# Kernel tuning notes

Measured on AMD Instinct MI355X. Metric: run time of the kernel, lower is better.

## Reference

```python
import jax, jax.numpy as jnp
import numpy as np

K_TOP = 64  # top-k selection size (init kwarg k)


def setup_inputs() -> dict:
    key = jax.random.key(0)
    k1, k2, k3, k4 = jax.random.split(key, 4)
    N, M, D = 512, 100000, 1024
    queries = jax.random.normal(k1, (N, D), dtype=jnp.float32)
    keys = jax.random.normal(k2, (M, D), dtype=jnp.float32)
    values = jax.random.normal(k3, (M, D), dtype=jnp.float32)
    affine = jax.random.normal(k4, (D,), dtype=jnp.float32)  # diag affine param (low_parameter=True)
    return {"queries": queries, "keys": keys, "values": values, "affine": affine}


def reference(queries, keys, values, affine):
    # low_parameter=True -> weight matrix is diag(affine): (queries @ diag(a)) == queries * a
    # scores[n, m] = (queries * affine) @ keys.T ; reduce max over queries dim (dim=0)
    scores = jnp.max(jnp.einsum('nd,md->nm', queries * affine, keys), axis=0)  # [M]
    weights, indices = jax.lax.top_k(scores, K_TOP)            # [k], [k]
    w = jax.nn.softmax(weights)                                # softmax over the k selected scores
    encoding = jnp.sum(w[:, None] * values[indices], axis=0)   # [V]
    return encoding, indices
```

## Files before the change

kernel.cpp:

```cpp
#include <hip/hip_runtime.h>
#include <cstdint>
#include <cstddef>


typedef __attribute__((ext_vector_type(8))) short bf16x8;
typedef __attribute__((ext_vector_type(4))) float f32x4;

static constexpr int NQ = 512;
static constexpr int DD = 1024;
static constexpr int MK = 100000;
static constexpr int BM = 64;
static constexpr int BK = 64;
static constexpr int NKS = DD / BK;
static constexpr int MBLOCKS = (MK + BM - 1) / BM;
static constexpr int CAP = 1024;

static constexpr size_t KSTAGE_OFF   = 0;
static constexpr size_t KSTAGE_BYTES = (size_t)MBLOCKS * NKS * BM * 128;
static constexpr size_t QSTAGE_OFF   = KSTAGE_OFF + KSTAGE_BYTES;
static constexpr size_t QSTAGE_BYTES = (size_t)NKS * NQ * 128;
static constexpr size_t SCORES_OFF   = QSTAGE_OFF + QSTAGE_BYTES;
static constexpr size_t SCORES_BYTES = (size_t)MBLOCKS * BM * sizeof(float);
static constexpr size_t CIDX_OFF     = SCORES_OFF + SCORES_BYTES;
static constexpr size_t RESC_OFF     = CIDX_OFF + (size_t)CAP * 4;
static constexpr size_t CNT_OFF      = RESC_OFF + (size_t)CAP * 4;
static constexpr size_t HIST_OFF     = CNT_OFF + 64;
static constexpr size_t VLO_OFF      = HIST_OFF + 8192 * 4;

static constexpr int AOFF = 0;
static constexpr int BOFF = 8192;
static constexpr int GEMM_LDS = 8192 + 65536;

static __device__ __forceinline__ unsigned short f32_to_bf16_rne(float f) {
    unsigned int u = __float_as_uint(f);
    unsigned int r = (u + 0x7FFFu + ((u >> 16) & 1u)) >> 16;
    return (unsigned short)r;
}
static __device__ __forceinline__ unsigned int xform(float f) {
    unsigned int u = __float_as_uint(f);
    return u ^ ((unsigned int)((int)u >> 31) | 0x80000000u);
}
static __device__ __forceinline__ float unxform(unsigned int u) {
    unsigned int b = (u & 0x80000000u) ? (u ^ 0x80000000u) : ~u;
    return __uint_as_float(b);
}

typedef __attribute__((address_space(1))) const unsigned int g1u32;
typedef __attribute__((address_space(3))) unsigned int l3u32;
static __device__ __forceinline__ void async16(const void* g, void* l) {
    __builtin_amdgcn_global_load_lds((g1u32*)g, (l3u32*)(uintptr_t)l, 16, 0, 0);
}

__global__ void prep_q(const float* __restrict__ q, const float* __restrict__ a,
                       unsigned short* __restrict__ qs) {
    int id  = blockIdx.x * 256 + threadIdx.x;
    int p   = id & 7;
    int row = (id >> 3) & (NQ - 1);
    int ks  = id >> 12;
    int c   = p ^ (row & 7);
    int kb  = ks * BK + c * 8;

    const float* qrow = q + (size_t)row * DD + kb;
    float4 v0 = *(const float4*)(qrow);
    float4 v1 = *(const float4*)(qrow + 4);
    float4 a0 = *(const float4*)(a + kb);
    float4 a1 = *(const float4*)(a + kb + 4);
    float f[8] = {v0.x * a0.x, v0.y * a0.y, v0.z * a0.z, v0.w * a0.w,
                  v1.x * a1.x, v1.y * a1.y, v1.z * a1.z, v1.w * a1.w};
    bf16x8 o;
#pragma unroll
    for (int j = 0; j < 8; ++j) o[j] = (short)f32_to_bf16_rne(f[j]);
    *(bf16x8*)(qs + (size_t)id * 8) = o;
}

__global__ void prep_keys(const float* __restrict__ keys,
                          unsigned short* __restrict__ kst) {
    size_t id = (size_t)blockIdx.x * 256 + threadIdx.x;
    int p   = (int)(id & 7);
    int row = (int)((id >> 3) & 63);
    int ks  = (int)((id >> 9) & 15);
    int mb  = (int)(id >> 13);
    int gm  = mb * 64 + row;
    bf16x8 o;
    if (gm < MK) {
        int col = ks * BK + (p ^ (row & 7)) * 8;
        const float* src = keys + (size_t)gm * DD + col;
        float4 v0 = *(const float4*)(src);
        float4 v1 = *(const float4*)(src + 4);
        float f[8] = {v0.x, v0.y, v0.z, v0.w, v1.x, v1.y, v1.z, v1.w};
#pragma unroll
        for (int j = 0; j < 8; ++j) o[j] = (short)f32_to_bf16_rne(f[j]);
    } else {
#pragma unroll
        for (int j = 0; j < 8; ++j) o[j] = 0;
    }
    *(bf16x8*)(kst + id * 8) = o;
}

__launch_bounds__(512, 4)
__global__ void scores_gemm(const unsigned short* __restrict__ kstage,
                            const unsigned short* __restrict__ qs,
                            float* __restrict__ scores) {
    extern __shared__ char smem[];
    const int tid  = threadIdx.x;
    const int wid  = tid >> 6;
    const int lane = tid & 63;
    const int g    = lane >> 4;
    const int r16  = lane & 15;

    const int nwg = gridDim.x;
    const int qq  = nwg >> 3, rr = nwg & 7;
    const int xcd = blockIdx.x & 7, loc = blockIdx.x >> 3;
    const int mb  = (xcd < rr ? xcd * (qq + 1) : rr * (qq + 1) + (xcd - rr) * qq) + loc;
    const int m0  = mb * BM;

    const char* asrc = (const char*)kstage + ((size_t)mb * NKS) * 8192
                     + wid * 1024 + lane * 16;
    const char* bsrc = (const char*)qs + (size_t)(wid * 64) * 128 + (size_t)lane * 16;

    int aoff[2][4], boff[2][4];
#pragma unroll
    for (int s = 0; s < 2; ++s) {
#pragma unroll
        for (int rt = 0; rt < 4; ++rt) {
            int row = rt * 16 + r16;
            aoff[s][rt] = AOFF + row * 128 + (((s * 4 + g) ^ (row & 7)) << 4);
        }
#pragma unroll
        for (int ct = 0; ct < 4; ++ct) {
            int row = wid * 64 + ct * 16 + r16;
            boff[s][ct] = BOFF + row * 128 + (((s * 4 + g) ^ (row & 7)) << 4);
        }
    }

    f32x4 acc[4][4] = {};

    for (int ks = 0; ks < NKS; ++ks) {
        async16(asrc + (size_t)ks * 8192, smem + AOFF + wid * 1024);
#pragma unroll
        for (int i = 0; i < 8; ++i)
            async16(bsrc + (size_t)ks * 65536 + i * 1024,
                    smem + BOFF + wid * 8192 + i * 1024);
        __syncthreads();

#pragma unroll
        for (int s = 0; s < 2; ++s) {
            bf16x8 ah[4], bh[4];
#pragma unroll
            for (int rt = 0; rt < 4; ++rt) ah[rt] = *(const bf16x8*)(smem + aoff[s][rt]);
#pragma unroll
            for (int ct = 0; ct < 4; ++ct) bh[ct] = *(const bf16x8*)(smem + boff[s][ct]);
#pragma unroll
            for (int rt = 0; rt < 4; ++rt)
#pragma unroll
                for (int ct = 0; ct < 4; ++ct)
                    acc[rt][ct] = __builtin_amdgcn_mfma_f32_16x16x32_bf16(ah[rt], bh[ct], acc[rt][ct], 0, 0, 0);
        }
        __syncthreads();
    }

    float* wmax = (float*)smem;
#pragma unroll
    for (int rt = 0; rt < 4; ++rt) {
#pragma unroll
        for (int r = 0; r < 4; ++r) {
            float mx = acc[rt][0][r];
            mx = fmaxf(mx, acc[rt][1][r]);
            mx = fmaxf(mx, acc[rt][2][r]);
            mx = fmaxf(mx, acc[rt][3][r]);
#pragma unroll
            for (int off = 1; off < 16; off <<= 1)
                mx = fmaxf(mx, __shfl_xor(mx, off));
            if (r16 == 0) wmax[wid * 64 + rt * 16 + g * 4 + r] = mx;
        }
    }
    __syncthreads();
    if (tid < BM) {
        float mx = wmax[tid];
#pragma unroll
        for (int w = 1; w < 8; ++w) mx = fmaxf(mx, wmax[w * 64 + tid]);
        int gm = m0 + tid;
        if (gm < MK) scores[gm] = mx;
    }
}

__global__ void zero_hist(unsigned int* __restrict__ hist, int* __restrict__ cnt) {
    int i = blockIdx.x * 1024 + threadIdx.x;
    if (i < 8192) hist[i] = 0;
    if (i == 0) cnt[0] = 0;
}

__global__ void hist_build(const float* __restrict__ scores, unsigned int* __restrict__ hist) {
    __shared__ unsigned int lh[8192];
    for (int i = threadIdx.x; i < 8192; i += 256) lh[i] = 0;
    __syncthreads();
    for (int i = blockIdx.x * 256 + threadIdx.x; i < MK; i += gridDim.x * 256)
        atomicAdd(&lh[xform(scores[i]) >> 19], 1u);
    __syncthreads();
    for (int i = threadIdx.x; i < 8192; i += 256) {
        unsigned int c = lh[i];
        if (c) atomicAdd(&hist[i], c);
    }
}

__launch_bounds__(1024)
__global__ void find_thresh(const unsigned int* __restrict__ hist, float* __restrict__ vlo) {
    __shared__ unsigned int s0[1024], s1[1024];
    const int tid = threadIdx.x;
    unsigned int s = 0;
#pragma unroll
    for (int j = 0; j < 8; ++j) s += hist[tid * 8 + j];
    s0[tid] = s;
    __syncthreads();
    unsigned int* src = s0;
    unsigned int* dst = s1;
    for (int off = 1; off < 1024; off <<= 1) {
        unsigned int v = src[tid] + ((tid + off < 1024) ? src[tid + off] : 0u);
        __syncthreads();
        dst[tid] = v;
        __syncthreads();
        unsigned int* t = src; src = dst; dst = t;
    }
    unsigned int suf  = src[tid];
    unsigned int sufn = (tid < 1023) ? src[tid + 1] : 0u;
    if (suf >= 64u && sufn < 64u) {
        unsigned int acc = sufn;
        int b = tid * 8 + 7;
        for (;; --b) { acc += hist[b]; if (acc >= 64u) break; }
        vlo[0] = unxform(((unsigned int)b) << 19) - 1.0f;
    }
}

__global__ void collect(const float* __restrict__ scores, const float* __restrict__ vlo,
                        int* __restrict__ cidx, int* __restrict__ cnt) {
    const float t = vlo[0];
    for (int i = blockIdx.x * 256 + threadIdx.x; i < MK; i += gridDim.x * 256) {
        if (scores[i] >= t) {
            int p = atomicAdd(cnt, 1);
            if (p < CAP) cidx[p] = i;
        }
    }
}

__launch_bounds__(256)
__global__ void rescore(const float* __restrict__ q, const float* __restrict__ a,
                        const float* __restrict__ keys,
                        const int* __restrict__ cidx, const int* __restrict__ cnt,
                        float* __restrict__ resc) {
    __shared__ float w[1024];
    __shared__ float smax[4];
    const int b = blockIdx.x;
    if (b >= cnt[0]) return;
    const int m   = cidx[b];
    const int tid = threadIdx.x;

    for (int d = tid; d < 1024; d += 256) w[d] = a[d] * keys[(size_t)m * DD + d];
    __syncthreads();

    const int wid = tid >> 6, lane = tid & 63;
    float best = -__builtin_inff();
    for (int n = wid; n < NQ; n += 4) {
        const float* qr = q + (size_t)n * DD;
        float p = 0.f;
#pragma unroll
        for (int j = 0; j < 4; ++j) {
            float4 v  = *(const float4*)(qr + lane * 4 + 256 * j);
            float4 ww = *(const float4*)(&w[lane * 4 + 256 * j]);
            p += v.x * ww.x + v.y * ww.y + v.z * ww.z + v.w * ww.w;
        }
#pragma unroll
        for (int off = 1; off < 64; off <<= 1) p += __shfl_xor(p, off);
        best = fmaxf(best, p);
    }
    if (lane == 0) smax[wid] = best;
    __syncthreads();
    if (tid == 0)
        resc[b] = fmaxf(fmaxf(smax[0], smax[1]), fmaxf(smax[2], smax[3]));
}

__launch_bounds__(256)
__global__ void final_select(const int* __restrict__ cidx, const float* __restrict__ resc,
                             const int* __restrict__ cnt, const float* __restrict__ values,
                             float* __restrict__ out) {
    __shared__ float selw[64];
    __shared__ int   seli[64];
    const int tid = threadIdx.x;
    int nc = cnt[0];
    if (nc > CAP) nc = CAP;

    if (tid < 64) {
        const int lane = tid;
        float lv[16]; int li[16];
#pragma unroll
        for (int j = 0; j < 16; ++j) {
            int slot = lane + 64 * j;
            bool ok = slot < nc;
            lv[j] = ok ? resc[slot] : -__builtin_inff();
            li[j] = ok ? cidx[slot] : 0x7fffffff;
        }
        for (int it = 0; it < 64; ++it) {
            float bv = -__builtin_inff();
            int bg = 0x7fffffff, bj = 0;
#pragma unroll
            for (int j = 0; j < 16; ++j)
                if (lv[j] > bv || (lv[j] == bv && li[j] < bg)) { bv = lv[j]; bg = li[j]; bj = j; }
            int bcode = (lane << 4) | bj;
#pragma unroll
            for (int off = 1; off < 64; off <<= 1) {
                float ov = __shfl_xor(bv, off);
                int   og = __shfl_xor(bg, off);
                int   oc = __shfl_xor(bcode, off);
                if (ov > bv || (ov == bv && og < bg)) { bv = ov; bg = og; bcode = oc; }
            }
            if ((bcode >> 4) == lane) {
                int wj = bcode & 15;
#pragma unroll
                for (int j = 0; j < 16; ++j) if (j == wj) lv[j] = -__builtin_inff();
            }
            if (lane == 0) { selw[it] = bv; seli[it] = bg; }
        }
    }
    __syncthreads();

    if (tid < 64) {
        float x = selw[tid];
        float mx = x;
#pragma unroll
        for (int off = 1; off < 64; off <<= 1) mx = fmaxf(mx, __shfl_xor(mx, off));
        float e = expf(x - mx);
        float s = e;
#pragma unroll
        for (int off = 1; off < 64; off <<= 1) s += __shfl_xor(s, off);
        selw[tid] = e / s;
        out[DD + tid] = (float)seli[tid];
    }
    __syncthreads();

    for (int d = tid; d < DD; d += 256) {
        float accv = 0.f;
        for (int i = 0; i < 64; ++i)
            accv += selw[i] * values[(size_t)seli[i] * DD + d];
        out[d] = accv;
    }
}

extern "C" void kernel_launch(void* const* d_in, const int* in_sizes, int n_in,
                              void* d_out, int out_size, void* d_ws, size_t ws_size,
                              hipStream_t stream) {
    (void)in_sizes; (void)n_in; (void)out_size; (void)ws_size;
    const float* queries = (const float*)d_in[0];
    const float* keys    = (const float*)d_in[1];
    const float* values  = (const float*)d_in[2];
    const float* affine  = (const float*)d_in[3];
    float* out = (float*)d_out;
    char*  ws  = (char*)d_ws;

    unsigned short* kstage = (unsigned short*)(ws + KSTAGE_OFF);
    unsigned short* qstage = (unsigned short*)(ws + QSTAGE_OFF);
    float* scores = (float*)(ws + SCORES_OFF);
    int*   cidx   = (int*)(ws + CIDX_OFF);
    float* resc   = (float*)(ws + RESC_OFF);
    int*   cnt    = (int*)(ws + CNT_OFF);
    unsigned int* hist = (unsigned int*)(ws + HIST_OFF);
    float* vlo    = (float*)(ws + VLO_OFF);

    hipFuncSetAttribute((const void*)scores_gemm,
                        hipFuncAttributeMaxDynamicSharedMemorySize, GEMM_LDS);

    prep_q<<<(NKS * NQ * 8) / 256, 256, 0, stream>>>(queries, affine, qstage);
    prep_keys<<<(MBLOCKS * NKS * BM * 8) / 256, 256, 0, stream>>>(keys, kstage);
    scores_gemm<<<MBLOCKS, 512, GEMM_LDS, stream>>>(kstage, qstage, scores);
    zero_hist<<<8, 1024, 0, stream>>>(hist, cnt);
    hist_build<<<64, 256, 0, stream>>>(scores, hist);
    find_thresh<<<1, 1024, 0, stream>>>(hist, vlo);
    collect<<<200, 256, 0, stream>>>(scores, vlo, cidx, cnt);
    rescore<<<CAP, 256, 0, stream>>>(queries, affine, keys, cidx, cnt, resc);
    final_select<<<1, 256, 0, stream>>>(cidx, resc, cnt, values, out);
}
```

Measured before the change: 534.5 us.

## Double-buffer larger GEMM tiles and add two-level histogram threshold

The scores GEMM now uses 128-row key tiles with double-buffered LDS for both operands, prefetching the next K step while MFMAs run on the current one, and raises wave priority around the MFMA block. Key and query staging layouts are rebuilt to match, with prep_keys using one 1024-thread block per tile. The top-k threshold search adds a fine histogram pass so the candidate threshold is much tighter, shrinking the number of rows that need exact fp32 rescoring. The trade-off is more LDS per block (lower occupancy), extra small kernels, and a tighter margin that the candidate set must still cover.

New measurement: 549.3 us. 2.8% more time.

```diff
diff --git a/kernel.cpp b/kernel.cpp
--- a/kernel.cpp
+++ b/kernel.cpp
@@ -9,27 +9,28 @@
 static constexpr int NQ = 512;
 static constexpr int DD = 1024;
 static constexpr int MK = 100000;
-static constexpr int BM = 64;
-static constexpr int BK = 64;
-static constexpr int NKS = DD / BK;
-static constexpr int MBLOCKS = (MK + BM - 1) / BM;
+static constexpr int BM = 128;
+static constexpr int KSTEPS = 16;
+static constexpr int MBLK = (MK + BM - 1) / BM;
 static constexpr int CAP = 1024;
 
 static constexpr size_t KSTAGE_OFF   = 0;
-static constexpr size_t KSTAGE_BYTES = (size_t)MBLOCKS * NKS * BM * 128;
+static constexpr size_t KSTAGE_BYTES = (size_t)MBLK * 262144;
 static constexpr size_t QSTAGE_OFF   = KSTAGE_OFF + KSTAGE_BYTES;
-static constexpr size_t QSTAGE_BYTES = (size_t)NKS * NQ * 128;
+static constexpr size_t QSTAGE_BYTES = (size_t)KSTEPS * 8 * NQ * 16;
 static constexpr size_t SCORES_OFF   = QSTAGE_OFF + QSTAGE_BYTES;
-static constexpr size_t SCORES_BYTES = (size_t)MBLOCKS * BM * sizeof(float);
+static constexpr size_t SCORES_BYTES = (size_t)MBLK * BM * 4;
 static constexpr size_t CIDX_OFF     = SCORES_OFF + SCORES_BYTES;
 static constexpr size_t RESC_OFF     = CIDX_OFF + (size_t)CAP * 4;
 static constexpr size_t CNT_OFF      = RESC_OFF + (size_t)CAP * 4;
-static constexpr size_t HIST_OFF     = CNT_OFF + 64;
-static constexpr size_t VLO_OFF      = HIST_OFF + 8192 * 4;
-
-static constexpr int AOFF = 0;
-static constexpr int BOFF = 8192;
-static constexpr int GEMM_LDS = 8192 + 65536;
+static constexpr size_t HISTC_OFF    = CNT_OFF + 64;
+static constexpr size_t HISTF_OFF    = HISTC_OFF + 8192 * 4;
+static constexpr size_t TB_OFF       = HISTF_OFF + 8192 * 4;
+static constexpr size_t VLO_OFF      = TB_OFF + 64;
+
+static constexpr int ABASE = 0;
+static constexpr int BBASE = 32768;
+static constexpr int GEMM_LDS = 32768 + 2 * 65536;
 
 static __device__ __forceinline__ unsigned short f32_to_bf16_rne(float f) {
     unsigned int u = __float_as_uint(f);
@@ -53,115 +54,129 @@
 
 __global__ void prep_q(const float* __restrict__ q, const float* __restrict__ a,
                        unsigned short* __restrict__ qs) {
-    int id  = blockIdx.x * 256 + threadIdx.x;
-    int p   = id & 7;
-    int row = (id >> 3) & (NQ - 1);
-    int ks  = id >> 12;
-    int c   = p ^ (row & 7);
-    int kb  = ks * BK + c * 8;
-
-    const float* qrow = q + (size_t)row * DD + kb;
+    int id = blockIdx.x * 256 + threadIdx.x;
+    int qq = id & 511;
+    int j  = (id >> 9) & 7;
+    int kk = id >> 12;
+    int col = kk * 64 + (j >> 2) * 32 + (j & 3) * 8;
+
+    const float* qrow = q + (size_t)qq * DD + col;
     float4 v0 = *(const float4*)(qrow);
     float4 v1 = *(const float4*)(qrow + 4);
-    float4 a0 = *(const float4*)(a + kb);
-    float4 a1 = *(const float4*)(a + kb + 4);
+    float4 a0 = *(const float4*)(a + col);
+    float4 a1 = *(const float4*)(a + col + 4);
     float f[8] = {v0.x * a0.x, v0.y * a0.y, v0.z * a0.z, v0.w * a0.w,
                   v1.x * a1.x, v1.y * a1.y, v1.z * a1.z, v1.w * a1.w};
     bf16x8 o;
 #pragma unroll
-    for (int j = 0; j < 8; ++j) o[j] = (short)f32_to_bf16_rne(f[j]);
+    for (int t = 0; t < 8; ++t) o[t] = (short)f32_to_bf16_rne(f[t]);
     *(bf16x8*)(qs + (size_t)id * 8) = o;
 }
 
+__launch_bounds__(1024)
 __global__ void prep_keys(const float* __restrict__ keys,
                           unsigned short* __restrict__ kst) {
-    size_t id = (size_t)blockIdx.x * 256 + threadIdx.x;
-    int p   = (int)(id & 7);
-    int row = (int)((id >> 3) & 63);
-    int ks  = (int)((id >> 9) & 15);
-    int mb  = (int)(id >> 13);
-    int gm  = mb * 64 + row;
-    bf16x8 o;
-    if (gm < MK) {
-        int col = ks * BK + (p ^ (row & 7)) * 8;
-        const float* src = keys + (size_t)gm * DD + col;
-        float4 v0 = *(const float4*)(src);
-        float4 v1 = *(const float4*)(src + 4);
-        float f[8] = {v0.x, v0.y, v0.z, v0.w, v1.x, v1.y, v1.z, v1.w};
-#pragma unroll
-        for (int j = 0; j < 8; ++j) o[j] = (short)f32_to_bf16_rne(f[j]);
-    } else {
-#pragma unroll
-        for (int j = 0; j < 8; ++j) o[j] = 0;
-    }
-    *(bf16x8*)(kst + id * 8) = o;
-}
-
-__launch_bounds__(512, 4)
+    const int mb = blockIdx.x;
+    const int t  = threadIdx.x;
+    char* const dst = (char*)kst + (size_t)mb * 262144;
+#pragma unroll
+    for (int it = 0; it < 16; ++it) {
+        const int idx  = it * 1024 + t;
+        const int row  = idx >> 7;
+        const int col8 = idx & 127;
+        const int gm   = mb * BM + row;
+        bf16x8 o;
+        if (gm < MK) {
+            const float* src = keys + (size_t)gm * DD + col8 * 8;
+            float4 v0 = *(const float4*)(src);
+            float4 v1 = *(const float4*)(src + 4);
+            o[0] = (short)f32_to_bf16_rne(v0.x);
+            o[1] = (short)f32_to_bf16_rne(v0.y);
+            o[2] = (short)f32_to_bf16_rne(v0.z);
+            o[3] = (short)f32_to_bf16_rne(v0.w);
+            o[4] = (short)f32_to_bf16_rne(v1.x);
+            o[5] = (short)f32_to_bf16_rne(v1.y);
+            o[6] = (short)f32_to_bf16_rne(v1.z);
+            o[7] = (short)f32_to_bf16_rne(v1.w);
+        } else {
+#pragma unroll
+            for (int k = 0; k < 8; ++k) o[k] = 0;
+        }
+        const int ks = col8 >> 3;
+        const int c  = col8 & 7;
+        *(bf16x8*)(dst + ks * 16384 + row * 128 + ((c ^ (row & 7)) << 4)) = o;
+    }
+}
+
+__launch_bounds__(512)
 __global__ void scores_gemm(const unsigned short* __restrict__ kstage,
                             const unsigned short* __restrict__ qs,
                             float* __restrict__ scores) {
     extern __shared__ char smem[];
-    const int tid  = threadIdx.x;
-    const int wid  = tid >> 6;
-    const int lane = tid & 63;
-    const int g    = lane >> 4;
-    const int r16  = lane & 15;
+    const int tid = threadIdx.x;
+    const int w   = tid >> 6;
+    const int l   = tid & 63;
+    const int g   = l >> 4;
+    const int r16 = l & 15;
 
     const int nwg = gridDim.x;
-    const int qq  = nwg >> 3, rr = nwg & 7;
+    const int qq8 = nwg >> 3, rr8 = nwg & 7;
     const int xcd = blockIdx.x & 7, loc = blockIdx.x >> 3;
-    const int mb  = (xcd < rr ? xcd * (qq + 1) : rr * (qq + 1) + (xcd - rr) * qq) + loc;
+    const int mb  = (xcd < rr8 ? xcd * (qq8 + 1) : rr8 * (qq8 + 1) + (xcd - rr8) * qq8) + loc;
     const int m0  = mb * BM;
 
-    const char* asrc = (const char*)kstage + ((size_t)mb * NKS) * 8192
-                     + wid * 1024 + lane * 16;
-    const char* bsrc = (const char*)qs + (size_t)(wid * 64) * 128 + (size_t)lane * 16;
-
-    int aoff[2][4], boff[2][4];
-#pragma unroll
-    for (int s = 0; s < 2; ++s) {
-#pragma unroll
-        for (int rt = 0; rt < 4; ++rt) {
-            int row = rt * 16 + r16;
-            aoff[s][rt] = AOFF + row * 128 + (((s * 4 + g) ^ (row & 7)) << 4);
-        }
-#pragma unroll
-        for (int ct = 0; ct < 4; ++ct) {
-            int row = wid * 64 + ct * 16 + r16;
-            boff[s][ct] = BOFF + row * 128 + (((s * 4 + g) ^ (row & 7)) << 4);
-        }
-    }
-
-    f32x4 acc[4][4] = {};
-
-    for (int ks = 0; ks < NKS; ++ks) {
-        async16(asrc + (size_t)ks * 8192, smem + AOFF + wid * 1024);
-#pragma unroll
-        for (int i = 0; i < 8; ++i)
-            async16(bsrc + (size_t)ks * 65536 + i * 1024,
-                    smem + BOFF + wid * 8192 + i * 1024);
+    const char* asrc = (const char*)kstage + (size_t)mb * 262144 + w * 2048 + l * 16;
+    const char* bsrc = (const char*)qs + (size_t)(w * 64 + l) * 16;
+
+    f32x4 acc[8][4] = {};
+
+#pragma unroll
+    for (int i = 0; i < 2; ++i)
+        async16(asrc + i * 1024, smem + ABASE + w * 2048 + i * 1024);
+#pragma unroll
+    for (int j = 0; j < 8; ++j)
+        async16(bsrc + (size_t)j * 8192, smem + BBASE + j * 8192 + w * 1024);
+    __syncthreads();
+
+    for (int t = 0; t < KSTEPS; ++t) {
+        const int cur = t & 1, nxt = cur ^ 1;
+        if (t + 1 < KSTEPS) {
+#pragma unroll
+            for (int i = 0; i < 2; ++i)
+                async16(asrc + (size_t)(t + 1) * 16384 + i * 1024,
+                        smem + ABASE + nxt * 16384 + w * 2048 + i * 1024);
+#pragma unroll
+            for (int j = 0; j < 8; ++j)
+                async16(bsrc + ((size_t)(t + 1) * 8 + j) * 8192,
+                        smem + BBASE + nxt * 65536 + j * 8192 + w * 1024);
+        }
+#pragma unroll
+        for (int s = 0; s < 2; ++s) {
+            const int c = s * 4 + g;
+            bf16x8 af[8], bfr[4];
+#pragma unroll
+            for (int rt = 0; rt < 8; ++rt)
+                af[rt] = *(const bf16x8*)(smem + ABASE + cur * 16384 +
+                    (rt * 16 + r16) * 128 + ((c ^ (r16 & 7)) << 4));
+#pragma unroll
+            for (int ct = 0; ct < 4; ++ct)
+                bfr[ct] = *(const bf16x8*)(smem + BBASE + cur * 65536 +
+                    c * 8192 + (w * 64 + ct * 16 + r16) * 16);
+            __builtin_amdgcn_s_setprio(1);
+#pragma unroll
+            for (int rt = 0; rt < 8; ++rt)
+#pragma unroll
+                for (int ct = 0; ct < 4; ++ct)
+                    acc[rt][ct] = __builtin_amdgcn_mfma_f32_16x16x32_bf16(
+                        af[rt], bfr[ct], acc[rt][ct], 0, 0, 0);
+            __builtin_amdgcn_s_setprio(0);
+        }
         __syncthreads();
-
-#pragma unroll
-        for (int s = 0; s < 2; ++s) {
-            bf16x8 ah[4], bh[4];
-#pragma unroll
-            for (int rt = 0; rt < 4; ++rt) ah[rt] = *(const bf16x8*)(smem + aoff[s][rt]);
-#pragma unroll
-            for (int ct = 0; ct < 4; ++ct) bh[ct] = *(const bf16x8*)(smem + boff[s][ct]);
-#pragma unroll
-            for (int rt = 0; rt < 4; ++rt)
-#pragma unroll
-                for (int ct = 0; ct < 4; ++ct)
-                    acc[rt][ct] = __builtin_amdgcn_mfma_f32_16x16x32_bf16(ah[rt], bh[ct], acc[rt][ct], 0, 0, 0);
-        }
-        __syncthreads();
     }
 
     float* wmax = (float*)smem;
 #pragma unroll
-    for (int rt = 0; rt < 4; ++rt) {
+    for (int rt = 0; rt < 8; ++rt) {
 #pragma unroll
         for (int r = 0; r < 4; ++r) {
             float mx = acc[rt][0][r];
@@ -171,22 +186,23 @@
 #pragma unroll
             for (int off = 1; off < 16; off <<= 1)
                 mx = fmaxf(mx, __shfl_xor(mx, off));
-            if (r16 == 0) wmax[wid * 64 + rt * 16 + g * 4 + r] = mx;
+            if (r16 == 0) wmax[w * 128 + rt * 16 + g * 4 + r] = mx;
         }
     }
     __syncthreads();
     if (tid < BM) {
         float mx = wmax[tid];
 #pragma unroll
-        for (int w = 1; w < 8; ++w) mx = fmaxf(mx, wmax[w * 64 + tid]);
+        for (int ww = 1; ww < 8; ++ww) mx = fmaxf(mx, wmax[ww * 128 + tid]);
         int gm = m0 + tid;
         if (gm < MK) scores[gm] = mx;
     }
 }
 
-__global__ void zero_hist(unsigned int* __restrict__ hist, int* __restrict__ cnt) {
+__global__ void zero_sel(unsigned int* __restrict__ hc, unsigned int* __restrict__ hf,
+                         int* __restrict__ cnt) {
     int i = blockIdx.x * 1024 + threadIdx.x;
-    if (i < 8192) hist[i] = 0;
+    if (i < 8192) { hc[i] = 0; hf[i] = 0; }
     if (i == 0) cnt[0] = 0;
 }
 
@@ -204,7 +220,7 @@
 }
 
 __launch_bounds__(1024)
-__global__ void find_thresh(const unsigned int* __restrict__ hist, float* __restrict__ vlo) {
+__global__ void find_coarse(const unsigned int* __restrict__ hist, int* __restrict__ tb) {
     __shared__ unsigned int s0[1024], s1[1024];
     const int tid = threadIdx.x;
     unsigned int s = 0;
@@ -224,10 +240,58 @@
     unsigned int suf  = src[tid];
     unsigned int sufn = (tid < 1023) ? src[tid + 1] : 0u;
     if (suf >= 64u && sufn < 64u) {
+        unsigned int acc = sufn, hb = 0;
+        int b = tid * 8 + 7;
+        for (;; --b) { hb = hist[b]; acc += hb; if (acc >= 64u) break; }
+        tb[0] = b;
+        tb[1] = (int)(acc - hb);
+    }
+}
+
+__global__ void hist_fine(const float* __restrict__ scores, const int* __restrict__ tb,
+                          unsigned int* __restrict__ fh) {
+    __shared__ unsigned int lh[8192];
+    for (int i = threadIdx.x; i < 8192; i += 256) lh[i] = 0;
+    __syncthreads();
+    const unsigned int b = (unsigned int)tb[0];
+    for (int i = blockIdx.x * 256 + threadIdx.x; i < MK; i += gridDim.x * 256) {
+        unsigned int u = xform(scores[i]);
+        if ((u >> 19) == b) atomicAdd(&lh[(u >> 6) & 8191u], 1u);
+    }
+    __syncthreads();
+    for (int i = threadIdx.x; i < 8192; i += 256) {
+        unsigned int c = lh[i];
+        if (c) atomicAdd(&fh[i], c);
+    }
+}
+
+__launch_bounds__(1024)
+__global__ void find_fine(const unsigned int* __restrict__ fh, const int* __restrict__ tb,
+                          float* __restrict__ vlo) {
+    __shared__ unsigned int s0[1024], s1[1024];
+    const int tid = threadIdx.x;
+    const unsigned int init = (unsigned int)tb[1];
+    unsigned int s = 0;
+#pragma unroll
+    for (int j = 0; j < 8; ++j) s += fh[tid * 8 + j];
+    s0[tid] = s;
+    __syncthreads();
+    unsigned int* src = s0;
+    unsigned int* dst = s1;
+    for (int off = 1; off < 1024; off <<= 1) {
+        unsigned int v = src[tid] + ((tid + off < 1024) ? src[tid + off] : 0u);
+        __syncthreads();
+        dst[tid] = v;
+        __syncthreads();
+        unsigned int* t = src; src = dst; dst = t;
+    }
+    unsigned int suf  = init + src[tid];
+    unsigned int sufn = init + ((tid < 1023) ? src[tid + 1] : 0u);
+    if (suf >= 64u && sufn < 64u) {
         unsigned int acc = sufn;
         int b = tid * 8 + 7;
-        for (;; --b) { acc += hist[b]; if (acc >= 64u) break; }
-        vlo[0] = unxform(((unsigned int)b) << 19) - 1.0f;
+        for (;; --b) { acc += fh[b]; if (acc >= 64u) break; }
+        vlo[0] = unxform(((unsigned int)tb[0] << 19) | ((unsigned int)b << 6)) - 0.8f;
     }
 }
 
@@ -247,14 +311,14 @@
                         const float* __restrict__ keys,
                         const int* __restrict__ cidx, const int* __restrict__ cnt,
                         float* __restrict__ resc) {
-    __shared__ float w[1024];
+    __shared__ float wsm[1024];
     __shared__ float smax[4];
     const int b = blockIdx.x;
     if (b >= cnt[0]) return;
     const int m   = cidx[b];
     const int tid = threadIdx.x;
 
-    for (int d = tid; d < 1024; d += 256) w[d] = a[d] * keys[(size_t)m * DD + d];
+    for (int d = tid; d < 1024; d += 256) wsm[d] = a[d] * keys[(size_t)m * DD + d];
     __syncthreads();
 
     const int wid = tid >> 6, lane = tid & 63;
@@ -265,7 +329,7 @@
 #pragma unroll
         for (int j = 0; j < 4; ++j) {
             float4 v  = *(const float4*)(qr + lane * 4 + 256 * j);
-            float4 ww = *(const float4*)(&w[lane * 4 + 256 * j]);
+            float4 ww = *(const float4*)(&wsm[lane * 4 + 256 * j]);
             p += v.x * ww.x + v.y * ww.y + v.z * ww.z + v.w * ww.w;
         }
 #pragma unroll
@@ -361,18 +425,22 @@
     int*   cidx   = (int*)(ws + CIDX_OFF);
     float* resc   = (float*)(ws + RESC_OFF);
     int*   cnt    = (int*)(ws + CNT_OFF);
-    unsigned int* hist = (unsigned int*)(ws + HIST_OFF);
+    unsigned int* hc = (unsigned int*)(ws + HISTC_OFF);
+    unsigned int* hf = (unsigned int*)(ws + HISTF_OFF);
+    int*   tb     = (int*)(ws + TB_OFF);
     float* vlo    = (float*)(ws + VLO_OFF);
 
     hipFuncSetAttribute((const void*)scores_gemm,
                         hipFuncAttributeMaxDynamicSharedMemorySize, GEMM_LDS);
 
-    prep_q<<<(NKS * NQ * 8) / 256, 256, 0, stream>>>(queries, affine, qstage);
-    prep_keys<<<(MBLOCKS * NKS * BM * 8) / 256, 256, 0, stream>>>(keys, kstage);
-    scores_gemm<<<MBLOCKS, 512, GEMM_LDS, stream>>>(kstage, qstage, scores);
-    zero_hist<<<8, 1024, 0, stream>>>(hist, cnt);
-    hist_build<<<64, 256, 0, stream>>>(scores, hist);
-    find_thresh<<<1, 1024, 0, stream>>>(hist, vlo);
+    prep_q<<<256, 256, 0, stream>>>(queries, affine, qstage);
+    prep_keys<<<MBLK, 1024, 0, stream>>>(keys, kstage);
+    scores_gemm<<<MBLK, 512, GEMM_LDS, stream>>>(kstage, qstage, scores);
+    zero_sel<<<8, 1024, 0, stream>>>(hc, hf, cnt);
+    hist_build<<<64, 256, 0, stream>>>(scores, hc);
+    find_coarse<<<1, 1024, 0, stream>>>(hc, tb);
+    hist_fine<<<64, 256, 0, stream>>>(scores, tb, hf);
+    find_fine<<<1, 1024, 0, stream>>>(hf, tb, vlo);
     collect<<<200, 256, 0, stream>>>(scores, vlo, cidx, cnt);
     rescore<<<CAP, 256, 0, stream>>>(queries, affine, keys, cidx, cnt, resc);
     final_select<<<1, 256, 0, stream>>>(cidx, resc, cnt, values, out);
```
